# Performance work log

Hardware: AMD Instinct MI355X
Metric: run time of the kernel (lower is better)

## Reference

```python
import jax, jax.numpy as jnp
import numpy as np

N = 100000       # nodes
E = 1600000      # edges (avg degree 16)
D_IN = 128
D_H = 128
N_CLS = 100      # = 25 * timesteps (timesteps=4)


def setup_inputs() -> dict:
    key = jax.random.key(0)
    ks = jax.random.split(key, 16)
    x = jax.random.normal(ks[0], (N, D_IN), dtype=jnp.float32)
    edge_index = jax.random.randint(ks[1], (2, E), 0, N, dtype=jnp.int64)

    def lin_w(k, fan_in, fan_out):
        return (jax.random.normal(k, (fan_in, fan_out), dtype=jnp.float32)
                / np.float32(np.sqrt(fan_in)))

    return {
        "x": x, "edge_index": edge_index,
        "W1": lin_w(ks[2], D_IN, D_H),  "b1": jnp.zeros((D_H,), jnp.float32),
        "W2": lin_w(ks[3], D_H, D_H),   "b2": jnp.zeros((D_H,), jnp.float32),
        "W3": lin_w(ks[4], D_H, D_H),   "b3": jnp.zeros((D_H,), jnp.float32),
        "W4": lin_w(ks[5], D_H, D_H),   "b4": jnp.zeros((D_H,), jnp.float32),
        "W5": lin_w(ks[6], D_H, N_CLS), "b5": jnp.zeros((N_CLS,), jnp.float32),
        "Wl": lin_w(ks[7], N_CLS, N_CLS), "bl": jnp.zeros((N_CLS,), jnp.float32),
    }


def _gcn_conv(x, W, b, src, dst, dinv):
    # PyG GCNConv: out = D^{-1/2} (A + I) D^{-1/2} (x W) + b
    h = x @ W                                        # [N, F_out]
    msg = h[src] * (dinv[src] * dinv[dst])[:, None]  # per-edge messages [E, F_out]
    agg = jax.ops.segment_sum(msg, dst, num_segments=N)
    agg = agg + h * (dinv * dinv)[:, None]           # self-loop term
    return agg + b


def reference(x, edge_index, W1, b1, W2, b2, W3, b3, W4, b4, W5, b5, Wl, bl):
    src, dst = edge_index[0], edge_index[1]
    # degrees including self-loop (edge weight 1)
    deg = jax.ops.segment_sum(jnp.ones((E,), x.dtype), dst, num_segments=N) + 1.0
    dinv = jax.lax.rsqrt(deg)

    h = jax.nn.relu(_gcn_conv(x, W1, b1, src, dst, dinv))
    h = _gcn_conv(h, W2, b2, src, dst, dinv)
    h = _gcn_conv(h, W3, b3, src, dst, dinv)
    h = _gcn_conv(h, W4, b4, src, dst, dinv)
    h = _gcn_conv(h, W5, b5, src, dst, dinv)
    # view(N, -1) is identity here ([N, N_CLS])
    return h @ Wl + bl
```

## Files before the change

### kernel.cpp

```cpp
#include <hip/hip_runtime.h>


typedef _Float16 h16;
typedef _Float16 __attribute__((ext_vector_type(4))) h16x4;
typedef _Float16 __attribute__((ext_vector_type(8))) h16x8;
typedef float __attribute__((ext_vector_type(4))) f32x4;

__global__ void k_detect(const int* __restrict__ edge, int* __restrict__ flag) {
  int t = threadIdx.x;
  if (edge[2 * t + 1] != 0) atomicOr(flag, 1);
}

static __device__ __forceinline__ int load_idx(const int* edge, const int* flag, size_t pos) {
  bool is64 = (*flag == 0);
  if (is64) return (int)((const long long*)edge)[pos];
  return edge[pos];
}

__global__ void k_count(const int* __restrict__ edge, const int* __restrict__ flag,
                        int* __restrict__ counts, int* __restrict__ rank,
                        int* __restrict__ dstc, int E) {
  int i = blockIdx.x * 256 + threadIdx.x;
  if (i >= E) return;
  int d = load_idx(edge, flag, (size_t)E + i);
  dstc[i] = d;
  rank[i] = atomicAdd(&counts[d], 1);
}

__global__ void k_chunksum(const int* __restrict__ counts, int* __restrict__ chunksums, int n) {
  __shared__ int sd[256];
  int t = threadIdx.x;
  int base = blockIdx.x * 1024 + t * 4;
  int s = 0;
#pragma unroll
  for (int j = 0; j < 4; ++j) { int i = base + j; if (i < n) s += counts[i]; }
  sd[t] = s; __syncthreads();
  for (int off = 128; off > 0; off >>= 1) {
    if (t < off) sd[t] += sd[t + off];
    __syncthreads();
  }
  if (t == 0) chunksums[blockIdx.x] = sd[0];
}

__global__ void k_root(const int* __restrict__ chunksums, int* __restrict__ chunkbase, int nchunks) {
  __shared__ int sc[128];
  int t = threadIdx.x;
  int v = (t < nchunks) ? chunksums[t] : 0;
  sc[t] = v; __syncthreads();
  for (int off = 1; off < 128; off <<= 1) {
    int x = (t >= off) ? sc[t - off] : 0;
    __syncthreads();
    sc[t] += x;
    __syncthreads();
  }
  if (t < nchunks) chunkbase[t] = sc[t] - v;
}

__global__ void k_scan3(const int* __restrict__ counts, const int* __restrict__ chunkbase,
                        int* __restrict__ offsets, float* __restrict__ dinv, int n, int E) {
  __shared__ int sd[256];
  int t = threadIdx.x;
  int base = blockIdx.x * 1024 + t * 4;
  int c[4]; int s = 0;
#pragma unroll
  for (int j = 0; j < 4; ++j) { int i = base + j; c[j] = (i < n) ? counts[i] : 0; s += c[j]; }
  sd[t] = s; __syncthreads();
  int v = s;
  for (int off = 1; off < 256; off <<= 1) {
    int x = (t >= off) ? sd[t - off] : 0;
    __syncthreads();
    sd[t] += x;
    __syncthreads();
  }
  int run = chunkbase[blockIdx.x] + sd[t] - v;
#pragma unroll
  for (int j = 0; j < 4; ++j) {
    int i = base + j;
    if (i < n) {
      offsets[i] = run;
      dinv[i] = rsqrtf((float)c[j] + 1.0f);
    }
    run += c[j];
  }
  if (blockIdx.x == 0 && t == 0) offsets[n] = E;
}

__global__ void k_fill(const int* __restrict__ edge, const int* __restrict__ flag,
                       const int* __restrict__ offsets, const int* __restrict__ rank,
                       const int* __restrict__ dstc, int* __restrict__ col, int E) {
  int i = blockIdx.x * 256 + threadIdx.x;
  if (i >= E) return;
  int s = load_idx(edge, flag, (size_t)i);
  int d = dstc[i];
  col[offsets[d] + rank[i]] = s;
}

__global__ void k_smm(const float* __restrict__ A, const float* __restrict__ B,
                      float* __restrict__ C, int M, int K, int Nc) {
  int idx = blockIdx.x * 256 + threadIdx.x;
  if (idx >= M * Nc) return;
  int i = idx / Nc, j = idx % Nc;
  float acc = 0.f;
  for (int k = 0; k < K; ++k) acc = fmaf(A[i * K + k], B[k * Nc + j], acc);
  C[idx] = acc;
}

__global__ void k_cvec(const float* __restrict__ b2, const float* __restrict__ b3,
                       const float* __restrict__ b4, const float* __restrict__ b5,
                       const float* __restrict__ bl, const float* __restrict__ Wl,
                       const float* __restrict__ R3, const float* __restrict__ R4,
                       const float* __restrict__ R5, float* __restrict__ corr) {
  int j = threadIdx.x;
  if (j >= 100) return;
  float a2 = 0.f, a3 = 0.f, a4 = 0.f, acb = 0.f;
  for (int k = 0; k < 128; ++k) {
    a2 = fmaf(b2[k], R3[k * 100 + j], a2);
    a3 = fmaf(b3[k], R4[k * 100 + j], a3);
    a4 = fmaf(b4[k], R5[k * 100 + j], a4);
  }
  for (int k = 0; k < 100; ++k) acb = fmaf(b5[k], Wl[k * 100 + j], acb);
  corr[j] = a2; corr[128 + j] = a3; corr[256 + j] = a4; corr[384 + j] = acb + bl[j];
}

template <typename TX, int M, int AUG>
__launch_bounds__(256)
__global__ void k_mm(const TX* __restrict__ X, const float* __restrict__ W,
                     const float* __restrict__ dinv, h16* __restrict__ out, int n) {
  const int K = 128, OS = 128;
  __shared__ h16 Xs[128 * 40];
  __shared__ h16 Wt[128 * 40];
  __shared__ float dv[128];
  int tid = threadIdx.x;
  int row0 = blockIdx.x * 128;
  int w = tid >> 6, lane = tid & 63;
  int lhi = lane >> 4, llo = lane & 15;

  if (tid < 128) dv[tid] = (row0 + tid < n) ? dinv[row0 + tid] : 0.f;

  f32x4 acc[2][8];
#pragma unroll
  for (int fr = 0; fr < 2; ++fr)
#pragma unroll
    for (int fc = 0; fc < 8; ++fc) {
      f32x4 z = {0.f, 0.f, 0.f, 0.f};
      acc[fr][fc] = z;
    }

  for (int kc = 0; kc < K; kc += 32) {
    __syncthreads();
    if (sizeof(TX) == 4) {
      for (int idx = tid * 4; idx < 128 * 32; idx += 1024) {
        int r = idx >> 5, c = idx & 31;
        f32x4 v = {0.f, 0.f, 0.f, 0.f};
        if (row0 + r < n)
          v = __builtin_nontemporal_load(
              (const f32x4*)&((const float*)X)[(size_t)(row0 + r) * K + kc + c]);
        h16x4 h = {(h16)v[0], (h16)v[1], (h16)v[2], (h16)v[3]};
        *(h16x4*)&Xs[r * 40 + c] = h;
      }
    } else {
      for (int idx = tid * 8; idx < 128 * 32; idx += 2048) {
        int r = idx >> 5, c = idx & 31;
        h16x8 v = {(h16)0.f, (h16)0.f, (h16)0.f, (h16)0.f,
                   (h16)0.f, (h16)0.f, (h16)0.f, (h16)0.f};
        if (row0 + r < n)
          v = __builtin_nontemporal_load(
              (const h16x8*)&((const h16*)X)[(size_t)(row0 + r) * K + kc + c]);
        *(h16x8*)&Xs[r * 40 + c] = v;
      }
    }
    for (int idx = tid * 4; idx < 32 * 128; idx += 1024) {
      int k = idx >> 7, nn = idx & 127;
      float4 v = make_float4(0.f, 0.f, 0.f, 0.f);
      if (nn < M) v = *(const float4*)&W[(size_t)(kc + k) * M + nn];
      Wt[(nn + 0) * 40 + k] = (h16)v.x;
      Wt[(nn + 1) * 40 + k] = (h16)v.y;
      Wt[(nn + 2) * 40 + k] = (h16)v.z;
      Wt[(nn + 3) * 40 + k] = (h16)v.w;
    }
    __syncthreads();

    h16x8 af0 = *(const h16x8*)&Xs[(w * 32 + llo) * 40 + lhi * 8];
    h16x8 af1 = *(const h16x8*)&Xs[(w * 32 + 16 + llo) * 40 + lhi * 8];
#pragma unroll
    for (int fc = 0; fc < 8; ++fc) {
      h16x8 bf = *(const h16x8*)&Wt[(fc * 16 + llo) * 40 + lhi * 8];
      acc[0][fc] = __builtin_amdgcn_mfma_f32_16x16x32_f16(af0, bf, acc[0][fc], 0, 0, 0);
      acc[1][fc] = __builtin_amdgcn_mfma_f32_16x16x32_f16(af1, bf, acc[1][fc], 0, 0, 0);
    }
  }

#pragma unroll
  for (int fr = 0; fr < 2; ++fr) {
#pragma unroll
    for (int r = 0; r < 4; ++r) {
      int lrow = w * 32 + fr * 16 + lhi * 4 + r;
      int grow = row0 + lrow;
      if (grow >= n) continue;
      float sc = dv[lrow];
#pragma unroll
      for (int fc = 0; fc < 8; ++fc) {
        int colj = fc * 16 + llo;
        float vv = (colj < M) ? acc[fr][fc][r] * sc
                 : ((AUG && colj == 100) ? sc : 0.f);
        out[(size_t)grow * OS + colj] = (h16)vv;
      }
    }
  }
}

template <int WIDTH, int MODE>
__global__ void k_agg(const h16* __restrict__ hs, const int* __restrict__ offsets,
                      const int* __restrict__ col, const float* __restrict__ dinv,
                      const float* __restrict__ bias, const float* __restrict__ corr,
                      void* __restrict__ out, int n, int fresh) {
  const int STRIDE = 128;
  int gw = (blockIdx.x * 256 + threadIdx.x) >> 6;
  int lane = threadIdx.x & 63;
  int half = lane >> 5, sl = lane & 31;
  int v = gw * 2 + half;
  int c = sl * 4;
  if (v >= n) return;
  if (c >= WIDTH) return;
  const h16* row = &hs[(size_t)v * STRIDE];
  h16x4 selfv = *(const h16x4*)&row[c];
  float a0 = (float)selfv[0], a1 = (float)selfv[1];
  float a2 = (float)selfv[2], a3 = (float)selfv[3];
  int s = offsets[v], e = offsets[v + 1];
  for (int i = s; i < e; i += 16) {
    h16x4 m[16];
#pragma unroll
    for (int j = 0; j < 16; ++j) {
      h16x4 z = {(h16)0.f, (h16)0.f, (h16)0.f, (h16)0.f};
      m[j] = z;
      if (i + j < e) {
        int u = col[i + j];
        m[j] = *(const h16x4*)&hs[(size_t)u * STRIDE + c];
      }
    }
#pragma unroll
    for (int j = 0; j < 16; ++j) {
      a0 += (float)m[j][0]; a1 += (float)m[j][1];
      a2 += (float)m[j][2]; a3 += (float)m[j][3];
    }
  }
  float w = dinv[v];
  if (MODE == 0) {
    float r0 = fmaxf(fmaf(a0, w, bias[c]),     0.f);
    float r1 = fmaxf(fmaf(a1, w, bias[c + 1]), 0.f);
    float r2 = fmaxf(fmaf(a2, w, bias[c + 2]), 0.f);
    float r3 = fmaxf(fmaf(a3, w, bias[c + 3]), 0.f);
    h16x4 p = {(h16)r0, (h16)r1, (h16)r2, (h16)r3};
    *(h16x4*)&((h16*)out)[(size_t)v * STRIDE + c] = p;
  } else if (MODE == 1) {
    float w2 = w * w;
    float r0 = a0 * w2, r1 = a1 * w2, r2 = a2 * w2, r3 = a3 * w2;
    if (c == fresh) r0 = w;
    else if (c + 1 == fresh) r1 = w;
    else if (c + 2 == fresh) r2 = w;
    else if (c + 3 == fresh) r3 = w;
    h16x4 p = {(h16)r0, (h16)r1, (h16)r2, (h16)r3};
    *(h16x4*)&((h16*)out)[(size_t)v * STRIDE + c] = p;
  } else {
    float inv_w = 1.0f / w;
    float v3 = (float)row[100] * inv_w;
    float v2 = (float)row[101] * inv_w;
    float v1 = (float)row[102] * inv_w;
    float r[4] = {a0, a1, a2, a3};
    float4 o;
    float* op = &o.x;
#pragma unroll
    for (int q = 0; q < 4; ++q) {
      op[q] = r[q] * w + v3 * corr[c + q] + v2 * corr[128 + c + q]
            + v1 * corr[256 + c + q] + corr[384 + c + q];
    }
    *(float4*)&((float*)out)[(size_t)v * 100 + c] = o;
  }
}

extern "C" void kernel_launch(void* const* d_in, const int* in_sizes, int n_in,
                              void* d_out, int out_size, void* d_ws, size_t ws_size,
                              hipStream_t stream) {
  const float* x    = (const float*)d_in[0];
  const int*   edge = (const int*)d_in[1];
  const float* W1 = (const float*)d_in[2];  const float* b1 = (const float*)d_in[3];
  const float* W2 = (const float*)d_in[4];  const float* b2 = (const float*)d_in[5];
  const float* W3 = (const float*)d_in[6];  const float* b3 = (const float*)d_in[7];
  const float* W4 = (const float*)d_in[8];  const float* b4 = (const float*)d_in[9];
  const float* W5 = (const float*)d_in[10]; const float* b5 = (const float*)d_in[11];
  const float* Wl = (const float*)d_in[12]; const float* bl = (const float*)d_in[13];

  const int N = in_sizes[0] / 128;
  const int E = in_sizes[1] / 2;

  char* ws = (char*)d_ws;
  size_t cur = 0;
  auto alloc = [&](size_t bytes) -> char* {
    char* p = ws + cur;
    cur = (cur + bytes + 255) & ~(size_t)255;
    return p;
  };
  int*    counts    = (int*)alloc((size_t)N * 4);
  int*    flag      = (int*)alloc(4);
  int*    offsets   = (int*)alloc((size_t)(N + 1) * 4);
  float*  dinv      = (float*)alloc((size_t)N * 4);
  int*    chunksums = (int*)alloc(128 * 4);
  int*    chunkbase = (int*)alloc(128 * 4);
  float*  R5        = (float*)alloc(128 * 100 * 4);
  float*  R4        = (float*)alloc(128 * 100 * 4);
  float*  R3        = (float*)alloc(128 * 100 * 4);
  float*  Wc        = (float*)alloc(128 * 100 * 4);
  float*  corr      = (float*)alloc(512 * 4);
  int*    rank      = (int*)alloc((size_t)E * 4);
  int*    dstc      = (int*)alloc((size_t)E * 4);
  int*    col       = (int*)alloc(((size_t)E + 16) * 4);
  h16*    bufA      = (h16*)alloc((size_t)N * 128 * 2);
  h16*    bufB      = (h16*)alloc((size_t)N * 128 * 2);
  (void)ws_size; (void)n_in; (void)out_size;

  hipMemsetAsync(counts, 0, (size_t)N * 4, stream);
  hipMemsetAsync(flag, 0, 4, stream);

  const int nchunks = (N + 1023) / 1024;
  const int egrid = (E + 255) / 256;

  k_detect<<<1, 256, 0, stream>>>(edge, flag);
  k_count<<<egrid, 256, 0, stream>>>(edge, flag, counts, rank, dstc, E);
  k_chunksum<<<nchunks, 256, 0, stream>>>(counts, chunksums, N);
  k_root<<<1, 128, 0, stream>>>(chunksums, chunkbase, nchunks);
  k_scan3<<<nchunks, 256, 0, stream>>>(counts, chunkbase, offsets, dinv, N, E);
  k_fill<<<egrid, 256, 0, stream>>>(edge, flag, offsets, rank, dstc, col, E);

  const int sgrid = (128 * 100 + 255) / 256;
  k_smm<<<sgrid, 256, 0, stream>>>(W5, Wl, R5, 128, 100, 100);
  k_smm<<<sgrid, 256, 0, stream>>>(W4, R5, R4, 128, 128, 100);
  k_smm<<<sgrid, 256, 0, stream>>>(W3, R4, R3, 128, 128, 100);
  k_smm<<<sgrid, 256, 0, stream>>>(W2, R3, Wc, 128, 128, 100);
  k_cvec<<<1, 128, 0, stream>>>(b2, b3, b4, b5, bl, Wl, R3, R4, R5, corr);

  const int mmgrid = (N + 127) / 128;
  const int agrid = (N + 7) / 8;

  k_mm<float, 128, 0><<<mmgrid, 256, 0, stream>>>(x, W1, dinv, bufA, N);
  k_agg<128, 0><<<agrid, 256, 0, stream>>>(bufA, offsets, col, dinv, b1, nullptr, bufB, N, 0);
  k_mm<h16, 100, 1><<<mmgrid, 256, 0, stream>>>(bufB, Wc, dinv, bufA, N);
  k_agg<104, 1><<<agrid, 256, 0, stream>>>(bufA, offsets, col, dinv, nullptr, nullptr, bufB, N, 101);
  k_agg<104, 1><<<agrid, 256, 0, stream>>>(bufB, offsets, col, dinv, nullptr, nullptr, bufA, N, 102);
  k_agg<104, 1><<<agrid, 256, 0, stream>>>(bufA, offsets, col, dinv, nullptr, nullptr, bufB, N, -1);
  k_agg<100, 2><<<agrid, 256, 0, stream>>>(bufB, offsets, col, dinv, nullptr, corr, (float*)d_out, N, -1);
}
```

Before: 693.1 us.

## Fuse weight-chain kernels into one block and prefetch neighbor indices in aggregation

The detect, four small-matmul and correction-vector launches are merged into a single 1024-thread block that keeps the right-hand matrix in shared memory, cutting five launches down to one. The aggregation loop now loads the next 16 column indices while gathering the current chunk, so the dependent index load is taken off the gather's critical path. The price is that the weight chain runs serially on one CU instead of across ~50 blocks, and the aggregation kernel uses more registers, which may lower occupancy.

After: 678.2 us. -2.2%, faster.

```diff
diff --git a/kernel.cpp b/kernel.cpp
--- a/kernel.cpp
+++ b/kernel.cpp
@@ -6,15 +6,73 @@
 typedef _Float16 __attribute__((ext_vector_type(8))) h16x8;
 typedef float __attribute__((ext_vector_type(4))) f32x4;
 
-__global__ void k_detect(const int* __restrict__ edge, int* __restrict__ flag) {
-  int t = threadIdx.x;
-  if (edge[2 * t + 1] != 0) atomicOr(flag, 1);
-}
-
 static __device__ __forceinline__ int load_idx(const int* edge, const int* flag, size_t pos) {
   bool is64 = (*flag == 0);
   if (is64) return (int)((const long long*)edge)[pos];
   return edge[pos];
+}
+
+__launch_bounds__(1024)
+__global__ void k_wchain(const int* __restrict__ edge, int* __restrict__ flag,
+                         const float* __restrict__ W2, const float* __restrict__ W3,
+                         const float* __restrict__ W4, const float* __restrict__ W5,
+                         const float* __restrict__ Wl,
+                         const float* __restrict__ b2, const float* __restrict__ b3,
+                         const float* __restrict__ b4, const float* __restrict__ b5,
+                         const float* __restrict__ bl,
+                         float* __restrict__ R5, float* __restrict__ R4,
+                         float* __restrict__ R3, float* __restrict__ Wc,
+                         float* __restrict__ corr) {
+  __shared__ float Bs[128 * 100];
+  int tid = threadIdx.x;
+  if (tid < 256 && edge[2 * tid + 1] != 0) atomicOr(flag, 1);
+  for (int idx = tid; idx < 100 * 100; idx += 1024) Bs[idx] = Wl[idx];
+  __syncthreads();
+  for (int idx = tid; idx < 12800; idx += 1024) {
+    int i = idx / 100, j = idx % 100;
+    float acc = 0.f;
+    for (int k = 0; k < 100; ++k) acc = fmaf(W5[i * 100 + k], Bs[k * 100 + j], acc);
+    R5[idx] = acc;
+  }
+  __syncthreads();
+  for (int idx = tid; idx < 12800; idx += 1024) Bs[idx] = R5[idx];
+  __syncthreads();
+  for (int idx = tid; idx < 12800; idx += 1024) {
+    int i = idx / 100, j = idx % 100;
+    float acc = 0.f;
+    for (int k = 0; k < 128; ++k) acc = fmaf(W4[i * 128 + k], Bs[k * 100 + j], acc);
+    R4[idx] = acc;
+  }
+  __syncthreads();
+  for (int idx = tid; idx < 12800; idx += 1024) Bs[idx] = R4[idx];
+  __syncthreads();
+  for (int idx = tid; idx < 12800; idx += 1024) {
+    int i = idx / 100, j = idx % 100;
+    float acc = 0.f;
+    for (int k = 0; k < 128; ++k) acc = fmaf(W3[i * 128 + k], Bs[k * 100 + j], acc);
+    R3[idx] = acc;
+  }
+  __syncthreads();
+  for (int idx = tid; idx < 12800; idx += 1024) Bs[idx] = R3[idx];
+  __syncthreads();
+  for (int idx = tid; idx < 12800; idx += 1024) {
+    int i = idx / 100, j = idx % 100;
+    float acc = 0.f;
+    for (int k = 0; k < 128; ++k) acc = fmaf(W2[i * 128 + k], Bs[k * 100 + j], acc);
+    Wc[idx] = acc;
+  }
+  __syncthreads();
+  if (tid < 100) {
+    int j = tid;
+    float a2 = 0.f, a3 = 0.f, a4 = 0.f, acb = 0.f;
+    for (int k = 0; k < 128; ++k) {
+      a2 = fmaf(b2[k], R3[k * 100 + j], a2);
+      a3 = fmaf(b3[k], R4[k * 100 + j], a3);
+      a4 = fmaf(b4[k], R5[k * 100 + j], a4);
+    }
+    for (int k = 0; k < 100; ++k) acb = fmaf(b5[k], Wl[k * 100 + j], acb);
+    corr[j] = a2; corr[128 + j] = a3; corr[256 + j] = a4; corr[384 + j] = acb + bl[j];
+  }
 }
 
 __global__ void k_count(const int* __restrict__ edge, const int* __restrict__ flag,
@@ -93,33 +151,6 @@
   int s = load_idx(edge, flag, (size_t)i);
   int d = dstc[i];
   col[offsets[d] + rank[i]] = s;
-}
-
-__global__ void k_smm(const float* __restrict__ A, const float* __restrict__ B,
-                      float* __restrict__ C, int M, int K, int Nc) {
-  int idx = blockIdx.x * 256 + threadIdx.x;
-  if (idx >= M * Nc) return;
-  int i = idx / Nc, j = idx % Nc;
-  float acc = 0.f;
-  for (int k = 0; k < K; ++k) acc = fmaf(A[i * K + k], B[k * Nc + j], acc);
-  C[idx] = acc;
-}
-
-__global__ void k_cvec(const float* __restrict__ b2, const float* __restrict__ b3,
-                       const float* __restrict__ b4, const float* __restrict__ b5,
-                       const float* __restrict__ bl, const float* __restrict__ Wl,
-                       const float* __restrict__ R3, const float* __restrict__ R4,
-                       const float* __restrict__ R5, float* __restrict__ corr) {
-  int j = threadIdx.x;
-  if (j >= 100) return;
-  float a2 = 0.f, a3 = 0.f, a4 = 0.f, acb = 0.f;
-  for (int k = 0; k < 128; ++k) {
-    a2 = fmaf(b2[k], R3[k * 100 + j], a2);
-    a3 = fmaf(b3[k], R4[k * 100 + j], a3);
-    a4 = fmaf(b4[k], R5[k * 100 + j], a4);
-  }
-  for (int k = 0; k < 100; ++k) acb = fmaf(b5[k], Wl[k * 100 + j], acb);
-  corr[j] = a2; corr[128 + j] = a3; corr[256 + j] = a4; corr[384 + j] = acb + bl[j];
 }
 
 template <typename TX, int M, int AUG>
@@ -227,22 +258,31 @@
   float a0 = (float)selfv[0], a1 = (float)selfv[1];
   float a2 = (float)selfv[2], a3 = (float)selfv[3];
   int s = offsets[v], e = offsets[v + 1];
+  int cc[16];
+#pragma unroll
+  for (int j = 0; j < 16; ++j) cc[j] = (s + j < e) ? col[s + j] : -1;
   for (int i = s; i < e; i += 16) {
+    int cn[16];
+#pragma unroll
+    for (int j = 0; j < 16; ++j) {
+      int idx = i + 16 + j;
+      cn[j] = (idx < e) ? col[idx] : -1;
+    }
     h16x4 m[16];
 #pragma unroll
     for (int j = 0; j < 16; ++j) {
       h16x4 z = {(h16)0.f, (h16)0.f, (h16)0.f, (h16)0.f};
       m[j] = z;
-      if (i + j < e) {
-        int u = col[i + j];
-        m[j] = *(const h16x4*)&hs[(size_t)u * STRIDE + c];
-      }
+      if (cc[j] >= 0)
+        m[j] = *(const h16x4*)&hs[(size_t)cc[j] * STRIDE + c];
     }
 #pragma unroll
     for (int j = 0; j < 16; ++j) {
       a0 += (float)m[j][0]; a1 += (float)m[j][1];
       a2 += (float)m[j][2]; a3 += (float)m[j][3];
     }
+#pragma unroll
+    for (int j = 0; j < 16; ++j) cc[j] = cn[j];
   }
   float w = dinv[v];
   if (MODE == 0) {
@@ -313,7 +353,7 @@
   float*  corr      = (float*)alloc(512 * 4);
   int*    rank      = (int*)alloc((size_t)E * 4);
   int*    dstc      = (int*)alloc((size_t)E * 4);
-  int*    col       = (int*)alloc(((size_t)E + 16) * 4);
+  int*    col       = (int*)alloc(((size_t)E + 32) * 4);
   h16*    bufA      = (h16*)alloc((size_t)N * 128 * 2);
   h16*    bufB      = (h16*)alloc((size_t)N * 128 * 2);
   (void)ws_size; (void)n_in; (void)out_size;
@@ -324,19 +364,13 @@
   const int nchunks = (N + 1023) / 1024;
   const int egrid = (E + 255) / 256;
 
-  k_detect<<<1, 256, 0, stream>>>(edge, flag);
+  k_wchain<<<1, 1024, 0, stream>>>(edge, flag, W2, W3, W4, W5, Wl,
+                                   b2, b3, b4, b5, bl, R5, R4, R3, Wc, corr);
   k_count<<<egrid, 256, 0, stream>>>(edge, flag, counts, rank, dstc, E);
   k_chunksum<<<nchunks, 256, 0, stream>>>(counts, chunksums, N);
   k_root<<<1, 128, 0, stream>>>(chunksums, chunkbase, nchunks);
   k_scan3<<<nchunks, 256, 0, stream>>>(counts, chunkbase, offsets, dinv, N, E);
   k_fill<<<egrid, 256, 0, stream>>>(edge, flag, offsets, rank, dstc, col, E);
-
-  const int sgrid = (128 * 100 + 255) / 256;
-  k_smm<<<sgrid, 256, 0, stream>>>(W5, Wl, R5, 128, 100, 100);
-  k_smm<<<sgrid, 256, 0, stream>>>(W4, R5, R4, 128, 128, 100);
-  k_smm<<<sgrid, 256, 0, stream>>>(W3, R4, R3, 128, 128, 100);
-  k_smm<<<sgrid, 256, 0, stream>>>(W2, R3, Wc, 128, 128, 100);
-  k_cvec<<<1, 128, 0, stream>>>(b2, b3, b4, b5, bl, Wl, R3, R4, R5, corr);
 
   const int mmgrid = (N + 127) / 128;
   const int agrid = (N + 7) / 8;
```
